# Performance work log

Hardware: AMD Instinct MI355X
Metric: run time of the kernel (lower is better)

## Reference

```python
import jax, jax.numpy as jnp
import numpy as np

B, I, O, C, U = 32, 2048, 32, 16, 32  # batch, in_channels(caps), out_capsules, in_capsules(dim), unit_size
NUM_ITERS = 3


def setup_inputs() -> dict:
    key = jax.random.key(0)
    k1, k2 = jax.random.split(key)
    x = jax.random.normal(k1, (B, I, C), dtype=jnp.float32)
    w = jax.random.normal(k2, (I, O, C, U), dtype=jnp.float32)
    return {"x": x, "w": w}


def _squash(v):
    # faithful to original: vec * |vec| / (1 + |vec|^2), norm over last (unit) dim
    n = jnp.linalg.norm(v, axis=-1, keepdims=True)
    return v * n / (1.0 + n * n)


def reference(x, w):
    # u_hat[b,i,o,u] = sum_c x[b,i,c] * w[i,o,c,u]   (the original's x @ w with singleton dims dropped)
    u_hat = jnp.einsum('bic,iocu->biou', x, w)  # [B,I,O,U]
    b_log = jnp.zeros((I, O, 1), dtype=x.dtype)
    v = None
    for _ in range(NUM_ITERS):
        # original computes softmax over dim=2 of [I,O,1] (a singleton dim) -> all ones; kept faithful
        c = jax.nn.softmax(b_log, axis=2)[..., 0]  # [I,O]
        s = jnp.einsum('io,biou->bou', c, u_hat)   # sum over input capsules
        v = _squash(s)                              # [B,O,U]
        # agreement: per-(b,i,o) dot(u_hat, v), then mean over batch (original's update.mean(dim=0))
        agree = jnp.einsum('biou,bou->io', u_hat, v) / B
        b_log = b_log + agree[..., None]
    return v[:, :, None, :]  # matches original v.squeeze(1) -> [B, O, 1, U]
```

## Files before the change

### kernel.cpp

```cpp
#include <hip/hip_runtime.h>
#include <math.h>

#define B_   32
#define I_   2048
#define O_   32
#define C_   16
#define U_   32
#define NCOL (O_ * U_)
#define TI   4
#define NBLK (I_ / TI)
#define SLICE (B_ * NCOL)
#define BH   16
#define XS   36


__global__ __launch_bounds__(512, 4) void caps_partial(const float* __restrict__ x,
                                                       const float* __restrict__ w,
                                                       float* __restrict__ ws) {
    __shared__ float xs[TI * C_ * XS];
    const int tid = threadIdx.x;
    const int i0 = blockIdx.x * TI;

    for (int k = tid; k < B_ * TI * C_; k += 512) {
        int b   = k >> 6;
        int rem = k & 63;
        xs[rem * XS + b] = x[(size_t)b * (I_ * C_) + (size_t)i0 * C_ + rem];
    }
    __syncthreads();

    const int bh = tid >> 8;
    const int ct = tid & 255;
    const int o  = ct >> 3;
    const int u4 = (ct & 7) << 2;
    const float* wp = w + (size_t)i0 * (O_ * C_ * U_) + o * (C_ * U_) + u4;

    float4 acc[BH];
#pragma unroll
    for (int b = 0; b < BH; ++b) acc[b] = make_float4(0.f, 0.f, 0.f, 0.f);

    for (int il = 0; il < TI; ++il) {
        const float* wpi = wp + (size_t)il * (O_ * C_ * U_);
        const float* xr  = &xs[il * C_ * XS + bh * BH];
#pragma unroll
        for (int cc = 0; cc < C_; cc += 4) {
            float4 wv[4];
#pragma unroll
            for (int j = 0; j < 4; ++j)
                wv[j] = *(const float4*)(wpi + (cc + j) * U_);
#pragma unroll
            for (int j = 0; j < 4; ++j) {
                const float4* xv = (const float4*)(xr + (cc + j) * XS);
#pragma unroll
                for (int q = 0; q < 4; ++q) {
                    float4 xq = xv[q];
                    float4* a = &acc[q * 4];
                    a[0].x = fmaf(xq.x, wv[j].x, a[0].x);
                    a[0].y = fmaf(xq.x, wv[j].y, a[0].y);
                    a[0].z = fmaf(xq.x, wv[j].z, a[0].z);
                    a[0].w = fmaf(xq.x, wv[j].w, a[0].w);
                    a[1].x = fmaf(xq.y, wv[j].x, a[1].x);
                    a[1].y = fmaf(xq.y, wv[j].y, a[1].y);
                    a[1].z = fmaf(xq.y, wv[j].z, a[1].z);
                    a[1].w = fmaf(xq.y, wv[j].w, a[1].w);
                    a[2].x = fmaf(xq.z, wv[j].x, a[2].x);
                    a[2].y = fmaf(xq.z, wv[j].y, a[2].y);
                    a[2].z = fmaf(xq.z, wv[j].z, a[2].z);
                    a[2].w = fmaf(xq.z, wv[j].w, a[2].w);
                    a[3].x = fmaf(xq.w, wv[j].x, a[3].x);
                    a[3].y = fmaf(xq.w, wv[j].y, a[3].y);
                    a[3].z = fmaf(xq.w, wv[j].z, a[3].z);
                    a[3].w = fmaf(xq.w, wv[j].w, a[3].w);
                }
            }
        }
    }

    float* op = ws + (size_t)blockIdx.x * SLICE + (size_t)(bh * BH) * NCOL + o * U_ + u4;
#pragma unroll
    for (int b = 0; b < BH; ++b)
        *(float4*)(op + (size_t)b * NCOL) = acc[b];
}

__global__ __launch_bounds__(256) void caps_reduce_squash(const float* __restrict__ ws,
                                                          float* __restrict__ out) {
    __shared__ float sh[128];
    const int tl = threadIdx.x & 127;
    const int ph = threadIdx.x >> 7;
    const int t  = blockIdx.x * 128 + tl;
    const float* p = ws + (size_t)ph * (NBLK / 2) * SLICE + t;
    float s = 0.f;
#pragma unroll 16
    for (int i = 0; i < NBLK / 2; ++i)
        s += p[(size_t)i * SLICE];
    if (ph) sh[tl] = s;
    __syncthreads();
    if (ph == 0) {
        s += sh[tl];
        float ss = s * s;
        ss += __shfl_xor(ss, 1);
        ss += __shfl_xor(ss, 2);
        ss += __shfl_xor(ss, 4);
        ss += __shfl_xor(ss, 8);
        ss += __shfl_xor(ss, 16);
        float n = sqrtf(ss);
        out[t] = s * n / (1.0f + ss);
    }
}

__global__ __launch_bounds__(256, 2) void caps_main_atomic(const float* __restrict__ x,
                                                           const float* __restrict__ w,
                                                           float* __restrict__ out) {
    __shared__ float xs[TI * C_ * 33];
    const int tid = threadIdx.x;
    const int i0 = blockIdx.x * TI;
    for (int k = tid; k < B_ * TI * C_; k += 256) {
        int b = k >> 6, rem = k & 63;
        xs[rem * 33 + b] = x[(size_t)b * (I_ * C_) + (size_t)i0 * C_ + rem];
    }
    __syncthreads();
    const int o = tid >> 3, u4 = (tid & 7) << 2;
    const float* wp = w + (size_t)i0 * (O_ * C_ * U_) + o * (C_ * U_) + u4;
    float4 acc[B_];
#pragma unroll
    for (int b = 0; b < B_; ++b) acc[b] = make_float4(0.f, 0.f, 0.f, 0.f);
    for (int il = 0; il < TI; ++il) {
        const float* wpi = wp + (size_t)il * (O_ * C_ * U_);
        const float* xr = &xs[il * C_ * 33];
#pragma unroll
        for (int c = 0; c < C_; ++c) {
            float4 wv = *(const float4*)(wpi + c * U_);
            const float* xc = xr + c * 33;
#pragma unroll
            for (int b = 0; b < B_; ++b) {
                float xb = xc[b];
                acc[b].x = fmaf(xb, wv.x, acc[b].x);
                acc[b].y = fmaf(xb, wv.y, acc[b].y);
                acc[b].z = fmaf(xb, wv.z, acc[b].z);
                acc[b].w = fmaf(xb, wv.w, acc[b].w);
            }
        }
    }
    float* op = out + o * U_ + u4;
#pragma unroll
    for (int b = 0; b < B_; ++b) {
        float* p = op + (size_t)b * NCOL;
        atomicAdd(p + 0, acc[b].x);
        atomicAdd(p + 1, acc[b].y);
        atomicAdd(p + 2, acc[b].z);
        atomicAdd(p + 3, acc[b].w);
    }
}

__global__ void caps_squash_inplace(float* __restrict__ out) {
    int t = blockIdx.x * 256 + threadIdx.x;
    float s = out[t];
    float ss = s * s;
    ss += __shfl_xor(ss, 1);
    ss += __shfl_xor(ss, 2);
    ss += __shfl_xor(ss, 4);
    ss += __shfl_xor(ss, 8);
    ss += __shfl_xor(ss, 16);
    float n = sqrtf(ss);
    out[t] = s * n / (1.0f + ss);
}

extern "C" void kernel_launch(void* const* d_in, const int* in_sizes, int n_in,
                              void* d_out, int out_size, void* d_ws, size_t ws_size,
                              hipStream_t stream) {
    const float* x = (const float*)d_in[0];
    const float* w = (const float*)d_in[1];
    float* out = (float*)d_out;

    const size_t need = (size_t)NBLK * SLICE * sizeof(float);
    if (ws_size >= need) {
        float* ws = (float*)d_ws;
        caps_partial<<<NBLK, 512, 0, stream>>>(x, w, ws);
        caps_reduce_squash<<<SLICE / 128, 256, 0, stream>>>(ws, out);
    } else {
        hipMemsetAsync(out, 0, (size_t)SLICE * sizeof(float), stream);
        caps_main_atomic<<<I_ / TI, 256, 0, stream>>>(x, w, out);
        caps_squash_inplace<<<SLICE / 256, 256, 0, stream>>>(out);
    }
}
```

Before: 212.6 us.

## Retile partial GEMM over more input capsules and split output capsules

Result: no change. 210.8 us (-0.8%).

```diff
diff --git a/kernel.cpp b/kernel.cpp
--- a/kernel.cpp
+++ b/kernel.cpp
@@ -7,10 +7,13 @@
 #define C_   16
 #define U_   32
 #define NCOL (O_ * U_)
-#define TI   4
-#define NBLK (I_ / TI)
-#define SLICE (B_ * NCOL)
-#define BH   16
+
+#define TI   8
+#define OSPL 2
+#define OH_  (O_ / OSPL)
+#define NIH  (I_ / TI)
+#define NBLK (NIH * OSPL)
+#define SLICE (B_ * OH_ * U_)
 #define XS   36
 
 
@@ -19,28 +22,31 @@
                                                        float* __restrict__ ws) {
     __shared__ float xs[TI * C_ * XS];
     const int tid = threadIdx.x;
-    const int i0 = blockIdx.x * TI;
+    const int ih  = blockIdx.x & (NIH - 1);
+    const int oh  = blockIdx.x >> 8;
+    const int i0  = ih * TI;
+    const int o0  = oh * OH_;
 
     for (int k = tid; k < B_ * TI * C_; k += 512) {
-        int b   = k >> 6;
-        int rem = k & 63;
+        int b   = k >> 7;
+        int rem = k & 127;
         xs[rem * XS + b] = x[(size_t)b * (I_ * C_) + (size_t)i0 * C_ + rem];
     }
     __syncthreads();
 
-    const int bh = tid >> 8;
-    const int ct = tid & 255;
-    const int o  = ct >> 3;
+    const int bh = tid >> 7;
+    const int ct = tid & 127;
+    const int oo = ct >> 3;
     const int u4 = (ct & 7) << 2;
-    const float* wp = w + (size_t)i0 * (O_ * C_ * U_) + o * (C_ * U_) + u4;
-
-    float4 acc[BH];
-#pragma unroll
-    for (int b = 0; b < BH; ++b) acc[b] = make_float4(0.f, 0.f, 0.f, 0.f);
+    const float* wp = w + (size_t)i0 * (O_ * C_ * U_) + (size_t)(o0 + oo) * (C_ * U_) + u4;
+
+    float4 acc[8];
+#pragma unroll
+    for (int b = 0; b < 8; ++b) acc[b] = make_float4(0.f, 0.f, 0.f, 0.f);
 
     for (int il = 0; il < TI; ++il) {
         const float* wpi = wp + (size_t)il * (O_ * C_ * U_);
-        const float* xr  = &xs[il * C_ * XS + bh * BH];
+        const float* xr  = &xs[(il * C_) * XS + bh * 8];
 #pragma unroll
         for (int cc = 0; cc < C_; cc += 4) {
             float4 wv[4];
@@ -49,36 +55,50 @@
                 wv[j] = *(const float4*)(wpi + (cc + j) * U_);
 #pragma unroll
             for (int j = 0; j < 4; ++j) {
-                const float4* xv = (const float4*)(xr + (cc + j) * XS);
-#pragma unroll
-                for (int q = 0; q < 4; ++q) {
-                    float4 xq = xv[q];
-                    float4* a = &acc[q * 4];
-                    a[0].x = fmaf(xq.x, wv[j].x, a[0].x);
-                    a[0].y = fmaf(xq.x, wv[j].y, a[0].y);
-                    a[0].z = fmaf(xq.x, wv[j].z, a[0].z);
-                    a[0].w = fmaf(xq.x, wv[j].w, a[0].w);
-                    a[1].x = fmaf(xq.y, wv[j].x, a[1].x);
-                    a[1].y = fmaf(xq.y, wv[j].y, a[1].y);
-                    a[1].z = fmaf(xq.y, wv[j].z, a[1].z);
-                    a[1].w = fmaf(xq.y, wv[j].w, a[1].w);
-                    a[2].x = fmaf(xq.z, wv[j].x, a[2].x);
-                    a[2].y = fmaf(xq.z, wv[j].y, a[2].y);
-                    a[2].z = fmaf(xq.z, wv[j].z, a[2].z);
-                    a[2].w = fmaf(xq.z, wv[j].w, a[2].w);
-                    a[3].x = fmaf(xq.w, wv[j].x, a[3].x);
-                    a[3].y = fmaf(xq.w, wv[j].y, a[3].y);
-                    a[3].z = fmaf(xq.w, wv[j].z, a[3].z);
-                    a[3].w = fmaf(xq.w, wv[j].w, a[3].w);
-                }
+                const float* xc = xr + (cc + j) * XS;
+                float4 xa = *(const float4*)(xc);
+                float4 xb = *(const float4*)(xc + 4);
+                acc[0].x = fmaf(xa.x, wv[j].x, acc[0].x);
+                acc[0].y = fmaf(xa.x, wv[j].y, acc[0].y);
+                acc[0].z = fmaf(xa.x, wv[j].z, acc[0].z);
+                acc[0].w = fmaf(xa.x, wv[j].w, acc[0].w);
+                acc[1].x = fmaf(xa.y, wv[j].x, acc[1].x);
+                acc[1].y = fmaf(xa.y, wv[j].y, acc[1].y);
+                acc[1].z = fmaf(xa.y, wv[j].z, acc[1].z);
+                acc[1].w = fmaf(xa.y, wv[j].w, acc[1].w);
+                acc[2].x = fmaf(xa.z, wv[j].x, acc[2].x);
+                acc[2].y = fmaf(xa.z, wv[j].y, acc[2].y);
+                acc[2].z = fmaf(xa.z, wv[j].z, acc[2].z);
+                acc[2].w = fmaf(xa.z, wv[j].w, acc[2].w);
+                acc[3].x = fmaf(xa.w, wv[j].x, acc[3].x);
+                acc[3].y = fmaf(xa.w, wv[j].y, acc[3].y);
+                acc[3].z = fmaf(xa.w, wv[j].z, acc[3].z);
+                acc[3].w = fmaf(xa.w, wv[j].w, acc[3].w);
+                acc[4].x = fmaf(xb.x, wv[j].x, acc[4].x);
+                acc[4].y = fmaf(xb.x, wv[j].y, acc[4].y);
+                acc[4].z = fmaf(xb.x, wv[j].z, acc[4].z);
+                acc[4].w = fmaf(xb.x, wv[j].w, acc[4].w);
+                acc[5].x = fmaf(xb.y, wv[j].x, acc[5].x);
+                acc[5].y = fmaf(xb.y, wv[j].y, acc[5].y);
+                acc[5].z = fmaf(xb.y, wv[j].z, acc[5].z);
+                acc[5].w = fmaf(xb.y, wv[j].w, acc[5].w);
+                acc[6].x = fmaf(xb.z, wv[j].x, acc[6].x);
+                acc[6].y = fmaf(xb.z, wv[j].y, acc[6].y);
+                acc[6].z = fmaf(xb.z, wv[j].z, acc[6].z);
+                acc[6].w = fmaf(xb.z, wv[j].w, acc[6].w);
+                acc[7].x = fmaf(xb.w, wv[j].x, acc[7].x);
+                acc[7].y = fmaf(xb.w, wv[j].y, acc[7].y);
+                acc[7].z = fmaf(xb.w, wv[j].z, acc[7].z);
+                acc[7].w = fmaf(xb.w, wv[j].w, acc[7].w);
             }
         }
     }
 
-    float* op = ws + (size_t)blockIdx.x * SLICE + (size_t)(bh * BH) * NCOL + o * U_ + u4;
-#pragma unroll
-    for (int b = 0; b < BH; ++b)
-        *(float4*)(op + (size_t)b * NCOL) = acc[b];
+    float* op = ws + (size_t)blockIdx.x * SLICE + (size_t)(bh * 8) * (OH_ * U_)
+                + oo * U_ + u4;
+#pragma unroll
+    for (int bl = 0; bl < 8; ++bl)
+        *(float4*)(op + (size_t)bl * (OH_ * U_)) = acc[bl];
 }
 
 __global__ __launch_bounds__(256) void caps_reduce_squash(const float* __restrict__ ws,
@@ -86,11 +106,17 @@
     __shared__ float sh[128];
     const int tl = threadIdx.x & 127;
     const int ph = threadIdx.x >> 7;
-    const int t  = blockIdx.x * 128 + tl;
-    const float* p = ws + (size_t)ph * (NBLK / 2) * SLICE + t;
+    const int e  = blockIdx.x * 128 + tl;
+    const int b  = e >> 10;
+    const int o  = (e >> 5) & 31;
+    const int u  = e & 31;
+    const int oh = o >> 4;
+    const int oo = o & 15;
+    const float* p = ws + (size_t)oh * NIH * SLICE + (size_t)ph * (NIH / 2) * SLICE
+                     + (size_t)b * (OH_ * U_) + oo * U_ + u;
     float s = 0.f;
 #pragma unroll 16
-    for (int i = 0; i < NBLK / 2; ++i)
+    for (int i = 0; i < NIH / 2; ++i)
         s += p[(size_t)i * SLICE];
     if (ph) sh[tl] = s;
     __syncthreads();
@@ -103,17 +129,18 @@
         ss += __shfl_xor(ss, 8);
         ss += __shfl_xor(ss, 16);
         float n = sqrtf(ss);
-        out[t] = s * n / (1.0f + ss);
-    }
-}
-
+        out[e] = s * n / (1.0f + ss);
+    }
+}
+
+#define FTI 4
 __global__ __launch_bounds__(256, 2) void caps_main_atomic(const float* __restrict__ x,
                                                            const float* __restrict__ w,
                                                            float* __restrict__ out) {
-    __shared__ float xs[TI * C_ * 33];
+    __shared__ float xs[FTI * C_ * 33];
     const int tid = threadIdx.x;
-    const int i0 = blockIdx.x * TI;
-    for (int k = tid; k < B_ * TI * C_; k += 256) {
+    const int i0 = blockIdx.x * FTI;
+    for (int k = tid; k < B_ * FTI * C_; k += 256) {
         int b = k >> 6, rem = k & 63;
         xs[rem * 33 + b] = x[(size_t)b * (I_ * C_) + (size_t)i0 * C_ + rem];
     }
@@ -123,7 +150,7 @@
     float4 acc[B_];
 #pragma unroll
     for (int b = 0; b < B_; ++b) acc[b] = make_float4(0.f, 0.f, 0.f, 0.f);
-    for (int il = 0; il < TI; ++il) {
+    for (int il = 0; il < FTI; ++il) {
         const float* wpi = wp + (size_t)il * (O_ * C_ * U_);
         const float* xr = &xs[il * C_ * 33];
 #pragma unroll
@@ -175,10 +202,10 @@
     if (ws_size >= need) {
         float* ws = (float*)d_ws;
         caps_partial<<<NBLK, 512, 0, stream>>>(x, w, ws);
-        caps_reduce_squash<<<SLICE / 128, 256, 0, stream>>>(ws, out);
+        caps_reduce_squash<<<(B_ * NCOL) / 128, 256, 0, stream>>>(ws, out);
     } else {
-        hipMemsetAsync(out, 0, (size_t)SLICE * sizeof(float), stream);
-        caps_main_atomic<<<I_ / TI, 256, 0, stream>>>(x, w, out);
-        caps_squash_inplace<<<SLICE / 256, 256, 0, stream>>>(out);
-    }
-}
+        hipMemsetAsync(out, 0, (size_t)(B_ * NCOL) * sizeof(float), stream);
+        caps_main_atomic<<<I_ / FTI, 256, 0, stream>>>(x, w, out);
+        caps_squash_inplace<<<(B_ * NCOL) / 256, 256, 0, stream>>>(out);
+    }
+}
```

## Double-buffer weight slices into LDS via async global_load_lds in partial kernel

Applied to the files above, without the earlier changes.

After: 247.8 us. +16.5%, slower.

```diff
diff --git a/kernel.cpp b/kernel.cpp
--- a/kernel.cpp
+++ b/kernel.cpp
@@ -1,5 +1,6 @@
 #include <hip/hip_runtime.h>
 #include <math.h>
+#include <stdint.h>
 
 #define B_   32
 #define I_   2048
@@ -7,19 +8,25 @@
 #define C_   16
 #define U_   32
 #define NCOL (O_ * U_)
+
 #define TI   4
 #define NBLK (I_ / TI)
 #define SLICE (B_ * NCOL)
-#define BH   16
+#define WSL  (O_ * C_ * U_)
 #define XS   36
 
-
-__global__ __launch_bounds__(512, 4) void caps_partial(const float* __restrict__ x,
+#define GLOAD_LDS16(gp, lp) \
+    __builtin_amdgcn_global_load_lds( \
+        (const __attribute__((address_space(1))) uint32_t*)(gp), \
+        (__attribute__((address_space(3))) uint32_t*)(lp), 16, 0, 0)
+
+__global__ __launch_bounds__(512, 2) void caps_partial(const float* __restrict__ x,
                                                        const float* __restrict__ w,
                                                        float* __restrict__ ws) {
+    __shared__ float wb[2][WSL];
     __shared__ float xs[TI * C_ * XS];
     const int tid = threadIdx.x;
-    const int i0 = blockIdx.x * TI;
+    const int i0  = blockIdx.x * TI;
 
     for (int k = tid; k < B_ * TI * C_; k += 512) {
         int b   = k >> 6;
@@ -28,57 +35,78 @@
     }
     __syncthreads();
 
-    const int bh = tid >> 8;
-    const int ct = tid & 255;
-    const int o  = ct >> 3;
-    const int u4 = (ct & 7) << 2;
-    const float* wp = w + (size_t)i0 * (O_ * C_ * U_) + o * (C_ * U_) + u4;
-
-    float4 acc[BH];
-#pragma unroll
-    for (int b = 0; b < BH; ++b) acc[b] = make_float4(0.f, 0.f, 0.f, 0.f);
-
+    const int lane  = tid & 63;
+    const int sbase = tid & ~63;
+
+    auto stage = [&](int il, float* buf) {
+        const float* gw = w + (size_t)(i0 + il) * WSL;
+#pragma unroll
+        for (int k = 0; k < 8; ++k) {
+            int s = sbase + k * 512 + lane;
+            GLOAD_LDS16(gw + (size_t)s * 4, buf + (size_t)s * 4);
+        }
+    };
+
+    const int bh  = tid >> 8;
+    const int ct  = tid & 255;
+    const int o   = ct >> 3;
+    const int u4i = ct & 7;
+
+    float4 acc[16];
+#pragma unroll
+    for (int m = 0; m < 16; ++m) acc[m] = make_float4(0.f, 0.f, 0.f, 0.f);
+
+    stage(0, wb[0]);
+
+#pragma unroll
     for (int il = 0; il < TI; ++il) {
-        const float* wpi = wp + (size_t)il * (O_ * C_ * U_);
-        const float* xr  = &xs[il * C_ * XS + bh * BH];
-#pragma unroll
-        for (int cc = 0; cc < C_; cc += 4) {
-            float4 wv[4];
-#pragma unroll
-            for (int j = 0; j < 4; ++j)
-                wv[j] = *(const float4*)(wpi + (cc + j) * U_);
-#pragma unroll
-            for (int j = 0; j < 4; ++j) {
-                const float4* xv = (const float4*)(xr + (cc + j) * XS);
-#pragma unroll
-                for (int q = 0; q < 4; ++q) {
-                    float4 xq = xv[q];
-                    float4* a = &acc[q * 4];
-                    a[0].x = fmaf(xq.x, wv[j].x, a[0].x);
-                    a[0].y = fmaf(xq.x, wv[j].y, a[0].y);
-                    a[0].z = fmaf(xq.x, wv[j].z, a[0].z);
-                    a[0].w = fmaf(xq.x, wv[j].w, a[0].w);
-                    a[1].x = fmaf(xq.y, wv[j].x, a[1].x);
-                    a[1].y = fmaf(xq.y, wv[j].y, a[1].y);
-                    a[1].z = fmaf(xq.y, wv[j].z, a[1].z);
-                    a[1].w = fmaf(xq.y, wv[j].w, a[1].w);
-                    a[2].x = fmaf(xq.z, wv[j].x, a[2].x);
-                    a[2].y = fmaf(xq.z, wv[j].y, a[2].y);
-                    a[2].z = fmaf(xq.z, wv[j].z, a[2].z);
-                    a[2].w = fmaf(xq.z, wv[j].w, a[2].w);
-                    a[3].x = fmaf(xq.w, wv[j].x, a[3].x);
-                    a[3].y = fmaf(xq.w, wv[j].y, a[3].y);
-                    a[3].z = fmaf(xq.w, wv[j].z, a[3].z);
-                    a[3].w = fmaf(xq.w, wv[j].w, a[3].w);
-                }
+        if (il + 1 < TI) {
+            stage(il + 1, wb[(il + 1) & 1]);
+            asm volatile("s_waitcnt vmcnt(8)" ::: "memory");
+        } else {
+            asm volatile("s_waitcnt vmcnt(0)" ::: "memory");
+        }
+        __builtin_amdgcn_s_barrier();
+        asm volatile("" ::: "memory");
+
+        const float* cb = wb[il & 1] + o * (C_ * U_) + u4i * 4;
+        const float* xr = xs + (il * C_) * XS + bh * 16;
+#pragma unroll
+        for (int c = 0; c < C_; ++c) {
+            float4 wv = *(const float4*)(cb + c * U_);
+            const float* xc = xr + c * XS;
+#pragma unroll
+            for (int q = 0; q < 4; ++q) {
+                float4 xq = *(const float4*)(xc + q * 4);
+                float4* a = acc + q * 4;
+                a[0].x = fmaf(xq.x, wv.x, a[0].x);
+                a[0].y = fmaf(xq.x, wv.y, a[0].y);
+                a[0].z = fmaf(xq.x, wv.z, a[0].z);
+                a[0].w = fmaf(xq.x, wv.w, a[0].w);
+                a[1].x = fmaf(xq.y, wv.x, a[1].x);
+                a[1].y = fmaf(xq.y, wv.y, a[1].y);
+                a[1].z = fmaf(xq.y, wv.z, a[1].z);
+                a[1].w = fmaf(xq.y, wv.w, a[1].w);
+                a[2].x = fmaf(xq.z, wv.x, a[2].x);
+                a[2].y = fmaf(xq.z, wv.y, a[2].y);
+                a[2].z = fmaf(xq.z, wv.z, a[2].z);
+                a[2].w = fmaf(xq.z, wv.w, a[2].w);
+                a[3].x = fmaf(xq.w, wv.x, a[3].x);
+                a[3].y = fmaf(xq.w, wv.y, a[3].y);
+                a[3].z = fmaf(xq.w, wv.z, a[3].z);
+                a[3].w = fmaf(xq.w, wv.w, a[3].w);
             }
         }
-    }
-
-    float* op = ws + (size_t)blockIdx.x * SLICE + (size_t)(bh * BH) * NCOL + o * U_ + u4;
-#pragma unroll
-    for (int b = 0; b < BH; ++b)
-        *(float4*)(op + (size_t)b * NCOL) = acc[b];
+
+        asm volatile("" ::: "memory");
+        __builtin_amdgcn_s_barrier();
+    }
+
+    float* op = ws + (size_t)blockIdx.x * SLICE + (size_t)(bh * 16) * NCOL
+                + o * U_ + u4i * 4;
+#pragma unroll
+    for (int m = 0; m < 16; ++m)
+        *(float4*)(op + (size_t)m * NCOL) = acc[m];
 }
 
 __global__ __launch_bounds__(256) void caps_reduce_squash(const float* __restrict__ ws,
@@ -107,13 +135,14 @@
     }
 }
 
+#define FTI 4
 __global__ __launch_bounds__(256, 2) void caps_main_atomic(const float* __restrict__ x,
                                                            const float* __restrict__ w,
                                                            float* __restrict__ out) {
-    __shared__ float xs[TI * C_ * 33];
+    __shared__ float xs[FTI * C_ * 33];
     const int tid = threadIdx.x;
-    const int i0 = blockIdx.x * TI;
-    for (int k = tid; k < B_ * TI * C_; k += 256) {
+    const int i0 = blockIdx.x * FTI;
+    for (int k = tid; k < B_ * FTI * C_; k += 256) {
         int b = k >> 6, rem = k & 63;
         xs[rem * 33 + b] = x[(size_t)b * (I_ * C_) + (size_t)i0 * C_ + rem];
     }
@@ -123,7 +152,7 @@
     float4 acc[B_];
 #pragma unroll
     for (int b = 0; b < B_; ++b) acc[b] = make_float4(0.f, 0.f, 0.f, 0.f);
-    for (int il = 0; il < TI; ++il) {
+    for (int il = 0; il < FTI; ++il) {
         const float* wpi = wp + (size_t)il * (O_ * C_ * U_);
         const float* xr = &xs[il * C_ * 33];
 #pragma unroll
@@ -177,8 +206,8 @@
         caps_partial<<<NBLK, 512, 0, stream>>>(x, w, ws);
         caps_reduce_squash<<<SLICE / 128, 256, 0, stream>>>(ws, out);
     } else {
-        hipMemsetAsync(out, 0, (size_t)SLICE * sizeof(float), stream);
-        caps_main_atomic<<<I_ / TI, 256, 0, stream>>>(x, w, out);
-        caps_squash_inplace<<<SLICE / 256, 256, 0, stream>>>(out);
-    }
-}
+        hipMemsetAsync(out, 0, (size_t)(B_ * NCOL) * sizeof(float), stream);
+        caps_main_atomic<<<I_ / FTI, 256, 0, stream>>>(x, w, out);
+        caps_squash_inplace<<<(B_ * NCOL) / 256, 256, 0, stream>>>(out);
+    }
+}
```
